# Kernel optimization log

Measured on AMD Instinct MI355X. Metric: run time of the kernel, lower is better.

The kernel has to match this reference:

```python
import jax, jax.numpy as jnp
import numpy as np

B, S, D = 4, 2048, 1024
N_HEAD = 16
D_HEAD = D // N_HEAD
WINDOW = 1024
D_FF = 4 * D
EPS = 1e-5
NEG = -1e10


def _layernorm(x, g, b):
    mu = jnp.mean(x, axis=-1, keepdims=True)
    var = jnp.mean(jnp.square(x - mu), axis=-1, keepdims=True)
    return (x - mu) * jax.lax.rsqrt(var + EPS) * g + b


def setup_inputs() -> dict:
    key = jax.random.key(0)
    ks = jax.random.split(key, 12)
    s = 1.0 / np.sqrt(D)
    x = jax.random.normal(ks[0], (B, S, D), dtype=jnp.float32)
    key_pad_mask = jax.random.bernoulli(ks[1], 0.1, (B, S))
    return {
        "x": x,
        "key_pad_mask": key_pad_mask,
        "ln1_g": jnp.ones((D,), jnp.float32),
        "ln1_b": jnp.zeros((D,), jnp.float32),
        "wq": jax.random.normal(ks[2], (D, D), jnp.float32) * s,
        "bq": jnp.zeros((D,), jnp.float32),
        "wkv": jax.random.normal(ks[3], (D, 2 * D), jnp.float32) * s,
        "bkv": jnp.zeros((2 * D,), jnp.float32),
        "ln2_g": jnp.ones((D,), jnp.float32),
        "ln2_b": jnp.zeros((D,), jnp.float32),
        "w1": jax.random.normal(ks[4], (D, D_FF), jnp.float32) * s,
        "b1": jnp.zeros((D_FF,), jnp.float32),
        "w2": jax.random.normal(ks[5], (D_FF, D), jnp.float32) * (1.0 / np.sqrt(D_FF)),
        "b2": jnp.zeros((D,), jnp.float32),
    }


def reference(x, key_pad_mask, ln1_g, ln1_b, wq, bq, wkv, bkv, ln2_g, ln2_b, w1, b1, w2, b2):
    ln1x = _layernorm(x, ln1_g, ln1_b)
    # queries over full sequence: [B, S, nh, dh]
    q = (ln1x @ wq + bq).reshape(B, S, N_HEAD, D_HEAD)
    # keys/values from the last WINDOW tokens: [B, W, 2*nh, dh]
    kv = (ln1x[:, -WINDOW:, :] @ wkv + bkv).reshape(B, WINDOW, 2 * N_HEAD, D_HEAD)
    k, v = kv[..., :N_HEAD, :], kv[..., N_HEAD:, :]
    # NOTE: original scales by sqrt(embed_dim), not sqrt(head_dim)
    scores = jnp.einsum('bqhd,bkhd->bhqk', q, k) / np.sqrt(D)
    causal = jnp.triu(jnp.ones((S, WINDOW), dtype=bool), k=1)  # faithful to original
    pad = key_pad_mask[:, None, None, -WINDOW:]
    scores = jnp.where(pad | causal[None, None], jnp.float32(NEG), scores)
    attn = jax.nn.softmax(scores, axis=-1)
    out = jnp.einsum('bhqk,bkhd->bqhd', attn, v).reshape(B, S, D)
    h = _layernorm(out, ln2_g, ln2_b)
    h = jax.nn.silu(h @ w1 + b1) @ w2 + b2
    return h + x
```

## Files before the change

### kernel.cpp

```cpp
#include <hip/hip_runtime.h>
#include <hip/hip_bf16.h>

#define BB 4
#define SS 2048
#define DD 1024
#define HH 16
#define DHH 64
#define WW 1024
#define DFF 4096
#define MM (BB*SS)
#define NEGV (-1e10f)
#define KSC 0.045084220027780106f

using f32x4 = __attribute__((ext_vector_type(4))) float;
using s16x8 = __attribute__((ext_vector_type(8))) short;
using s16x4 = __attribute__((ext_vector_type(4))) short;
using u64 = unsigned long long;

typedef const __attribute__((address_space(1))) void* gas_t;
typedef __attribute__((address_space(3))) void* las_t;

__device__ inline short f2b(float f) {
  __hip_bfloat16 h = __float2bfloat16(f);
  return __builtin_bit_cast(short, h);
}
__device__ inline float b2f(short u) {
  __hip_bfloat16 h = __builtin_bit_cast(__hip_bfloat16, u);
  return __bfloat162float(h);
}

__device__ inline void gload_lds16(const short* g, short* lds) {
  __builtin_amdgcn_global_load_lds((gas_t)g, (las_t)lds, 16, 0, 0);
}

__device__ inline f32x4 mfma16(s16x8 a, s16x8 b, f32x4 c) {
  return __builtin_amdgcn_mfma_f32_16x16x32_bf16(a, b, c, 0, 0, 0);
}

template<int IN_BF16>
__global__ __launch_bounds__(256) void ln_kernel(const void* __restrict__ inp,
                                                 const float* __restrict__ g,
                                                 const float* __restrict__ bta,
                                                 short* __restrict__ outp) {
  int row = blockIdx.x;
  int t = threadIdx.x;
  float v[4];
  if constexpr (IN_BF16) {
    s16x4 r4 = *((const s16x4*)((const short*)inp + (size_t)row*DD) + t);
    v[0]=b2f(r4[0]); v[1]=b2f(r4[1]); v[2]=b2f(r4[2]); v[3]=b2f(r4[3]);
  } else {
    f32x4 r4 = *((const f32x4*)((const float*)inp + (size_t)row*DD) + t);
    v[0]=r4[0]; v[1]=r4[1]; v[2]=r4[2]; v[3]=r4[3];
  }
  float s = v[0]+v[1]+v[2]+v[3];
  float sq = v[0]*v[0]+v[1]*v[1]+v[2]*v[2]+v[3]*v[3];
  for (int m=1;m<64;m<<=1){ s += __shfl_xor(s,m); sq += __shfl_xor(sq,m); }
  __shared__ float red[8];
  int wv = t>>6;
  if ((t&63)==0){ red[wv]=s; red[4+wv]=sq; }
  __syncthreads();
  s  = red[0]+red[1]+red[2]+red[3];
  sq = red[4]+red[5]+red[6]+red[7];
  float mean = s*(1.f/DD);
  float rstd = rsqrtf(sq*(1.f/DD) - mean*mean + 1e-5f);
  int col = t*4;
  s16x4 o;
  #pragma unroll
  for (int j=0;j<4;++j) o[j] = f2b((v[j]-mean)*rstd*g[col+j]+bta[col+j]);
  *((s16x4*)(outp + (size_t)row*DD) + t) = o;
}

__global__ __launch_bounds__(256) void transpose_cast(const float* __restrict__ in,
                                                      short* __restrict__ out,
                                                      int K, int N) {
  __shared__ float tile[32][33];
  int n0 = blockIdx.x*32, k0 = blockIdx.y*32;
  int tx = threadIdx.x & 31, ty = threadIdx.x >> 5;
  #pragma unroll
  for (int j=0;j<4;++j) tile[ty+8*j][tx] = in[(size_t)(k0+ty+8*j)*N + n0+tx];
  __syncthreads();
  #pragma unroll
  for (int j=0;j<4;++j) out[(size_t)(n0+ty+8*j)*K + k0+tx] = f2b(tile[tx][ty+8*j]);
}

__global__ void pad_bitmask(const int* __restrict__ pad, u64* __restrict__ pm) {
  int idx = threadIdx.x;
  int b_ = idx>>4, col = idx&15;
  const int* pb = pad + b_*SS + (SS-WW);
  u64 m = 0;
  for (int c=0;c<16;++c)
    for (int nf=0;nf<4;++nf)
      if (pb[c*64+nf*16+col]) m |= (1ull << (c*4+nf));
  pm[idx] = m;
}

template<int EPI>
__global__ __launch_bounds__(256) void gemm_bt(const short* __restrict__ A,
                                               const short* __restrict__ Bt,
                                               const float* __restrict__ bias,
                                               void* __restrict__ out1,
                                               void* __restrict__ out2,
                                               const float* __restrict__ resid,
                                               int N, int K, int lgx) {
  __shared__ short As[128*32], Bs[128*32];
  int tid = threadIdx.x, l = tid&63;
  int wv = tid>>6, wm = wv>>1, wn = wv&1;
  int q8 = gridDim.x >> 3;
  int wg = (blockIdx.x & 7)*q8 + (blockIdx.x >> 3);
  int bx = wg & ((1<<lgx)-1), by = wg >> lgx;
  const short* Ablk;
  if constexpr (EPI==1) {
    int b_ = (by*128)>>10;
    int w0 = (by*128)&1023;
    Ablk = A + ((size_t)b_*SS + (SS-WW) + w0)*DD;
  } else {
    Ablk = A + (size_t)by*128*K;
  }
  const short* Bblk = Bt + (size_t)bx*128*K;
  f32x4 acc[4][4];
  #pragma unroll
  for (int i=0;i<4;++i)
    #pragma unroll
    for(int j=0;j<4;++j)
      #pragma unroll
      for(int r=0;r<4;++r) acc[i][j][r]=0.f;
  int rA = l & 15;
  int cslot = (((l>>4) ^ ((l>>1)&3))*8);
  for (int kt=0; kt<K; kt+=32) {
    __syncthreads();
    #pragma unroll
    for (int p=0;p<2;++p) {
      int s = p*256 + tid;
      int srow = s>>2;
      int scs = (((s&3) ^ ((s>>3)&3))*8);
      gload_lds16(Ablk + (size_t)srow*K + kt + scs, &As[(p*256 + (tid & ~63))*8]);
      gload_lds16(Bblk + (size_t)srow*K + kt + scs, &Bs[(p*256 + (tid & ~63))*8]);
    }
    __syncthreads();
    s16x8 af[4], bfr[4];
    #pragma unroll
    for (int mf=0;mf<4;++mf) af[mf]  = *(const s16x8*)&As[(wm*64+mf*16+rA)*32 + cslot];
    #pragma unroll
    for (int nf=0;nf<4;++nf) bfr[nf] = *(const s16x8*)&Bs[(wn*64+nf*16+rA)*32 + cslot];
    #pragma unroll
    for (int mf=0;mf<4;++mf)
      #pragma unroll
      for (int nf=0;nf<4;++nf)
        acc[mf][nf] = mfma16(af[mf], bfr[nf], acc[mf][nf]);
  }
  #pragma unroll
  for (int mf=0;mf<4;++mf) {
    #pragma unroll
    for (int nf=0;nf<4;++nf) {
      #pragma unroll
      for (int r=0;r<4;++r) {
        int row = by*128 + wm*64 + mf*16 + ((l>>4)<<2) + r;
        int col = bx*128 + wn*64 + nf*16 + (l&15);
        float v = acc[mf][nf][r] + bias[col];
        if constexpr (EPI==0) {
          ((short*)out1)[(size_t)row*N + col] = f2b(v);
        } else if constexpr (EPI==1) {
          int b_ = row>>10, w_ = row&1023;
          if (col < DD) {
            int h = col>>6, dh = col&63;
            ((short*)out1)[(((size_t)(b_*HH+h))*WW + w_)*DHH + dh] = f2b(v*KSC);
          } else {
            int cc = col - DD;
            int h = cc>>6, dh = cc&63;
            ((short*)out2)[(((size_t)(b_*HH+h))*DHH + dh)*WW + w_] = f2b(v);
          }
        } else if constexpr (EPI==2) {
          float sv = v / (1.f + __expf(-v));
          ((short*)out1)[(size_t)row*N + col] = f2b(sv);
        } else {
          ((float*)out1)[(size_t)row*N + col] = v + resid[(size_t)row*N + col];
        }
      }
    }
  }
}

struct KF { s16x8 v[4][2]; };

__global__ __launch_bounds__(64,2) void attn_kernel(const short* __restrict__ q,
    const short* __restrict__ kpan, const short* __restrict__ vtpan,
    const u64* __restrict__ pmarr, short* __restrict__ outp) {
  __shared__ short P[32*72];
  int l = threadIdx.x;
  int id = blockIdx.x;
  int xcd = id & 7, slot = id >> 3;
  int bh = xcd + 8*(slot >> 6);
  int u  = 63 - (slot & 63);
  int bb = bh >> 4, h = bh & 15;
  int r0 = u*32;
  const short* kbase = kpan + (size_t)bh*WW*DHH;
  const short* vbase = vtpan + (size_t)bh*DHH*WW;
  u64 pmask = pmarr[bb*16 + (l&15)];
  const s16x8 ones8 = { 0x3F80,0x3F80,0x3F80,0x3F80,0x3F80,0x3F80,0x3F80,0x3F80 };

  s16x8 aq[2][2];
  #pragma unroll
  for (int g=0;g<2;++g)
    #pragma unroll
    for (int kf=0;kf<2;++kf)
      aq[g][kf] = *(const s16x8*)(q + ((size_t)bb*SS + r0 + g*16 + (l&15))*DD
                                    + h*DHH + (l>>4)*8 + kf*32);
  f32x4 oacc[2][4];
  float mrun[2][4], lrun[2][4], scale[2][4];
  #pragma unroll
  for (int g=0;g<2;++g)
    #pragma unroll
    for (int i=0;i<4;++i) {
      #pragma unroll
      for (int r=0;r<4;++r) oacc[g][i][r]=0.f;
      mrun[g][i]=-INFINITY; lrun[g][i]=0.f;
    }
  int dchunk = u>>1;
  int nch = dchunk+1 < 16 ? dchunk+1 : 16;

  auto loadK = [&](int c, KF& d) {
    const short* kc = kbase + (size_t)c*64*DHH;
    #pragma unroll
    for (int nf=0;nf<4;++nf) {
      const short* p = kc + (size_t)(nf*16+(l&15))*DHH + ((l>>4)*8);
      d.v[nf][0] = *(const s16x8*)p;
      d.v[nf][1] = *(const s16x8*)(p+32);
    }
  };

  auto body = [&](int c, KF& kf) {
    f32x4 sc[2][4];
    #pragma unroll
    for (int g=0;g<2;++g)
      #pragma unroll
      for (int nf=0;nf<4;++nf)
        #pragma unroll
        for (int r=0;r<4;++r) sc[g][nf][r]=0.f;
    __builtin_amdgcn_s_setprio(1);
    #pragma unroll
    for (int nf=0;nf<4;++nf)
      #pragma unroll
      for (int g=0;g<2;++g) {
        sc[g][nf] = mfma16(aq[g][0], kf.v[nf][0], sc[g][nf]);
        sc[g][nf] = mfma16(aq[g][1], kf.v[nf][1], sc[g][nf]);
      }
    __builtin_amdgcn_s_setprio(0);
    unsigned nib = (unsigned)(pmask >> (c*4)) & 15u;
    float pm[2][4];
    #pragma unroll
    for (int g=0;g<2;++g)
      #pragma unroll
      for (int r=0;r<4;++r) pm[g][r] = -INFINITY;
    if (c >= dchunk) {
      #pragma unroll
      for (int nf=0;nf<4;++nf) {
        int j = c*64 + nf*16 + (l&15);
        int padj = (int)((nib>>nf)&1u);
        #pragma unroll
        for (int g=0;g<2;++g)
          #pragma unroll
          for (int r=0;r<4;++r) {
            int sq_ = r0 + g*16 + ((l>>4)<<2) + r;
            float xv = (padj || (j > sq_)) ? NEGV : sc[g][nf][r];
            sc[g][nf][r] = xv;
            pm[g][r] = fmaxf(pm[g][r], xv);
          }
      }
    } else {
      #pragma unroll
      for (int nf=0;nf<4;++nf) {
        int padj = (int)((nib>>nf)&1u);
        #pragma unroll
        for (int g=0;g<2;++g)
          #pragma unroll
          for (int r=0;r<4;++r) {
            float xv = padj ? NEGV : sc[g][nf][r];
            sc[g][nf][r] = xv;
            pm[g][r] = fmaxf(pm[g][r], xv);
          }
      }
    }
    s16x8 vf0[4], vf1[4];
    #pragma unroll
    for (int nf=0;nf<4;++nf)
      vf0[nf] = *(const s16x8*)(vbase + (size_t)(nf*16+(l&15))*WW
                                + c*64 + ((l>>4)*8));
    int need = 0;
    #pragma unroll
    for (int g=0;g<2;++g)
      #pragma unroll
      for (int r=0;r<4;++r) need |= (pm[g][r] > mrun[g][r] + 12.f) ? 1 : 0;
    #pragma unroll
    for (int g=0;g<2;++g)
      #pragma unroll
      for (int r=0;r<4;++r) scale[g][r] = 1.f;
    if (__any(need)) {
      #pragma unroll
      for (int m=1;m<16;m<<=1)
        #pragma unroll
        for (int g=0;g<2;++g)
          #pragma unroll
          for (int r=0;r<4;++r) pm[g][r] = fmaxf(pm[g][r], __shfl_xor(pm[g][r], m));
      #pragma unroll
      for (int g=0;g<2;++g)
        #pragma unroll
        for (int r=0;r<4;++r) {
          float mn = fmaxf(mrun[g][r], pm[g][r]);
          scale[g][r] = exp2f(mrun[g][r]-mn);
          mrun[g][r] = mn;
        }
      #pragma unroll
      for (int g=0;g<2;++g)
        #pragma unroll
        for (int nf=0;nf<4;++nf)
          #pragma unroll
          for (int r=0;r<4;++r) oacc[g][nf][r] *= scale[g][r];
    }
    #pragma unroll
    for (int nf=0;nf<4;++nf)
      #pragma unroll
      for (int g=0;g<2;++g)
        #pragma unroll
        for (int r=0;r<4;++r)
          sc[g][nf][r] = exp2f(sc[g][nf][r]-mrun[g][r]);
    #pragma unroll
    for (int nf=0;nf<4;++nf)
      vf1[nf] = *(const s16x8*)(vbase + (size_t)(nf*16+(l&15))*WW
                                + c*64 + 32 + ((l>>4)*8));
    #pragma unroll
    for (int g=0;g<2;++g)
      #pragma unroll
      for (int nf=0;nf<4;++nf)
        #pragma unroll
        for (int r=0;r<4;++r)
          P[(g*16+((l>>4)<<2)+r)*72 + nf*16 + (l&15)] = f2b(sc[g][nf][r]);
    f32x4 ls2[2];
    #pragma unroll
    for (int g=0;g<2;++g)
      #pragma unroll
      for (int r=0;r<4;++r) ls2[g][r]=0.f;
    __builtin_amdgcn_s_setprio(1);
    #pragma unroll
    for (int ks=0;ks<2;++ks) {
      s16x8 ap[2];
      #pragma unroll
      for (int g=0;g<2;++g) {
        ap[g] = *(const s16x8*)&P[(g*16+(l&15))*72 + ks*32 + ((l>>4)*8)];
        ls2[g] = mfma16(ap[g], ones8, ls2[g]);
      }
      #pragma unroll
      for (int nf=0;nf<4;++nf) {
        s16x8 bv = ks ? vf1[nf] : vf0[nf];
        #pragma unroll
        for (int g=0;g<2;++g)
          oacc[g][nf] = mfma16(ap[g], bv, oacc[g][nf]);
      }
    }
    __builtin_amdgcn_s_setprio(0);
    #pragma unroll
    for (int g=0;g<2;++g)
      #pragma unroll
      for (int r=0;r<4;++r) lrun[g][r] = lrun[g][r]*scale[g][r] + ls2[g][r];
  };

  KF ka, kb;
  loadK(0, ka);
  int cend = nch, c = 0, ext = 0;
  while (true) {
    if (c == cend) {
      if (ext) break;
      ext = 1;
      int dead = 0;
      #pragma unroll
      for (int g=0;g<2;++g)
        #pragma unroll
        for (int r=0;r<4;++r) dead |= (mrun[g][r] < -5e9f) ? 1 : 0;
      if (!__any(dead)) break;
      cend = 16;
      if (c >= 16) break;
    }
    if (c+1 < 16) loadK(c+1, kb);
    body(c, ka);
    ka = kb;
    ++c;
  }

  #pragma unroll
  for (int g=0;g<2;++g)
    #pragma unroll
    for (int nf=0;nf<4;++nf)
      #pragma unroll
      for (int r=0;r<4;++r) {
        int srow = r0 + g*16 + ((l>>4)<<2) + r;
        float o = oacc[g][nf][r] / lrun[g][r];
        outp[((size_t)bb*SS + srow)*DD + h*DHH + nf*16 + (l&15)] = f2b(o);
      }
}

extern "C" void kernel_launch(void* const* d_in, const int* in_sizes, int n_in,
                              void* d_out, int out_size, void* d_ws, size_t ws_size,
                              hipStream_t stream) {
  const float* x    = (const float*)d_in[0];
  const int*   pad  = (const int*)d_in[1];
  const float* ln1g = (const float*)d_in[2];
  const float* ln1b = (const float*)d_in[3];
  const float* wq   = (const float*)d_in[4];
  const float* bq   = (const float*)d_in[5];
  const float* wkv  = (const float*)d_in[6];
  const float* bkv  = (const float*)d_in[7];
  const float* ln2g = (const float*)d_in[8];
  const float* ln2b = (const float*)d_in[9];
  const float* w1   = (const float*)d_in[10];
  const float* b1   = (const float*)d_in[11];
  const float* w2   = (const float*)d_in[12];
  const float* b2   = (const float*)d_in[13];

  char* ws = (char*)d_ws;
  const size_t MB = 1024*1024;
  short* ln1x = (short*)(ws + 0);
  short* qb   = (short*)(ws + 16*MB);
  short* kpan = (short*)(ws + 32*MB);
  short* vtp  = (short*)(ws + 40*MB);
  u64*   pmar = (u64*)  (ws + 48*MB);
  short* h1   = (short*)(ws + 0);
  short* outb = (short*)(ws + 64*MB);
  short* hb   = (short*)(ws + 80*MB);
  short* wqT  = (short*)(ws + 96*MB);
  short* wkvT = (short*)(ws + 98*MB);
  short* w1T  = (short*)(ws + 102*MB);
  short* w2T  = (short*)(ws + 110*MB);

  pad_bitmask<<<1,64,0,stream>>>(pad, pmar);
  transpose_cast<<<dim3(32,32),  256,0,stream>>>(wq,  wqT,  1024, 1024);
  transpose_cast<<<dim3(64,32),  256,0,stream>>>(wkv, wkvT, 1024, 2048);
  transpose_cast<<<dim3(128,32), 256,0,stream>>>(w1,  w1T,  1024, 4096);
  transpose_cast<<<dim3(32,128), 256,0,stream>>>(w2,  w2T,  4096, 1024);
  ln_kernel<0><<<MM,256,0,stream>>>(x, ln1g, ln1b, ln1x);
  gemm_bt<0><<<512, 256,0,stream>>>(ln1x, wqT,  bq,  qb,   nullptr, nullptr, 1024, 1024, 3);
  gemm_bt<1><<<512, 256,0,stream>>>(ln1x, wkvT, bkv, kpan, vtp,     nullptr, 2048, 1024, 4);
  attn_kernel<<<4096,64,0,stream>>>(qb, kpan, vtp, pmar, outb);
  ln_kernel<1><<<MM,256,0,stream>>>(outb, ln2g, ln2b, hb);
  gemm_bt<2><<<2048,256,0,stream>>>(hb, w1T, b1, h1,    nullptr, nullptr, 4096, 1024, 5);
  gemm_bt<3><<<512, 256,0,stream>>>(h1, w2T, b2, d_out, nullptr, x,       1024, 4096, 3);
}
```

Baseline: 437.4 us.

## Add 256x256-tile pipelined GEMM kernel for the FFN up-projection

```diff
diff --git a/kernel.cpp b/kernel.cpp
--- a/kernel.cpp
+++ b/kernel.cpp
@@ -180,6 +180,115 @@
   }
 }
 
+template<int EPI>
+__global__ __launch_bounds__(512,2) void gemm256(const short* __restrict__ A,
+                                                 const short* __restrict__ Bt,
+                                                 const float* __restrict__ bias,
+                                                 void* __restrict__ out1,
+                                                 int N, int K, int lgx) {
+  __shared__ short lds[32768];
+  int tid = threadIdx.x, l = tid&63, wid = tid>>6;
+  int wm = wid>>2, wn = wid&3;
+  int q8 = gridDim.x >> 3;
+  int wg = (blockIdx.x & 7)*q8 + (blockIdx.x >> 3);
+  int bx = wg & ((1<<lgx)-1), by = wg >> lgx;
+  const short* Ablk = A + (size_t)by*256*K;
+  const short* Bblk = Bt + (size_t)bx*256*K;
+  int rA = l & 15;
+  int slot_s = ((l>>4) ^ ((rA>>1)&3))*8;
+  int aBase = (wm*128 + rA)*32 + slot_s;
+  int bBase = (wn*64  + rA)*32 + slot_s + 8192;
+  int qs = (tid&3) ^ ((tid>>3)&3);
+  const short* srcA = Ablk + (size_t)(tid>>2)*K + qs*8;
+  const short* srcB = Bblk + (size_t)(tid>>2)*K + qs*8;
+  int dst0 = (tid & ~63)*8;
+  int nt = K >> 5;
+  f32x4 acc[8][4];
+  #pragma unroll
+  for (int i=0;i<8;++i)
+    #pragma unroll
+    for (int j=0;j<4;++j)
+      #pragma unroll
+      for (int r=0;r<4;++r) acc[i][j][r]=0.f;
+
+  auto stage = [&](int isB, int b, int t) {
+    const short* s = isB ? srcB : srcA;
+    short* d = &lds[b*16384 + isB*8192 + dst0];
+    gload_lds16(s + t*32,                 d);
+    gload_lds16(s + (size_t)128*K + t*32, d + 4096);
+  };
+  s16x8 af[4], bf[4];
+  auto readA = [&](int b, int mg) {
+    #pragma unroll
+    for (int j=0;j<4;++j) af[j] = *(const s16x8*)&lds[b*16384 + aBase + (mg*4+j)*512];
+  };
+  auto readB = [&](int b) {
+    #pragma unroll
+    for (int j=0;j<4;++j) bf[j] = *(const s16x8*)&lds[b*16384 + bBase + j*512];
+  };
+  auto mfmas = [&](int mg) {
+    __builtin_amdgcn_s_setprio(1);
+    #pragma unroll
+    for (int j=0;j<4;++j)
+      #pragma unroll
+      for (int nf=0;nf<4;++nf)
+        acc[mg*4+j][nf] = mfma16(af[j], bf[nf], acc[mg*4+j][nf]);
+    __builtin_amdgcn_s_setprio(0);
+  };
+
+  stage(0,0,0); stage(1,0,0); stage(1,1,1);
+  asm volatile("s_waitcnt vmcnt(2)" ::: "memory");
+  __builtin_amdgcn_s_barrier();
+
+  for (int it = 0; it < (nt>>1); ++it) {
+    int t0 = 2*it;
+    int t2 = t0+2; if (t2 >= nt) t2 -= nt;
+    int t3 = t0+3; if (t3 >= nt) t3 -= nt;
+    readB(0); readA(0,0);
+    stage(0,1,t0+1);
+    __builtin_amdgcn_s_barrier();
+    mfmas(0);
+    __builtin_amdgcn_s_barrier();
+    readA(0,1);
+    stage(1,0,t2);
+    __builtin_amdgcn_s_barrier();
+    mfmas(1);
+    asm volatile("s_waitcnt vmcnt(2)" ::: "memory");
+    __builtin_amdgcn_s_barrier();
+    readB(1); readA(1,0);
+    stage(0,0,t2);
+    __builtin_amdgcn_s_barrier();
+    mfmas(0);
+    __builtin_amdgcn_s_barrier();
+    readA(1,1);
+    stage(1,1,t3);
+    __builtin_amdgcn_s_barrier();
+    mfmas(1);
+    asm volatile("s_waitcnt vmcnt(2)" ::: "memory");
+    __builtin_amdgcn_s_barrier();
+  }
+  asm volatile("s_waitcnt vmcnt(0)" ::: "memory");
+
+  #pragma unroll
+  for (int mf=0;mf<8;++mf) {
+    #pragma unroll
+    for (int nf=0;nf<4;++nf) {
+      #pragma unroll
+      for (int r=0;r<4;++r) {
+        int row = by*256 + wm*128 + mf*16 + ((l>>4)<<2) + r;
+        int col = bx*256 + wn*64 + nf*16 + rA;
+        float v = acc[mf][nf][r] + bias[col];
+        if constexpr (EPI==2) {
+          float sv = v / (1.f + __expf(-v));
+          ((short*)out1)[(size_t)row*N + col] = f2b(sv);
+        } else {
+          ((short*)out1)[(size_t)row*N + col] = f2b(v);
+        }
+      }
+    }
+  }
+}
+
 struct KF { s16x8 v[4][2]; };
 
 __global__ __launch_bounds__(64,2) void attn_kernel(const short* __restrict__ q,
@@ -440,6 +549,6 @@
   gemm_bt<1><<<512, 256,0,stream>>>(ln1x, wkvT, bkv, kpan, vtp,     nullptr, 2048, 1024, 4);
   attn_kernel<<<4096,64,0,stream>>>(qb, kpan, vtp, pmar, outb);
   ln_kernel<1><<<MM,256,0,stream>>>(outb, ln2g, ln2b, hb);
-  gemm_bt<2><<<2048,256,0,stream>>>(hb, w1T, b1, h1,    nullptr, nullptr, 4096, 1024, 5);
+  gemm256<2><<<512,512,0,stream>>>(hb, w1T, b1, h1, 4096, 1024, 4);
   gemm_bt<3><<<512, 256,0,stream>>>(h1, w2T, b2, d_out, nullptr, x,       1024, 4096, 3);
 }
```

Measured after the change: 403.4 us. -7.8%, faster.
